# Kernel optimization log

Measured on AMD Instinct MI355X. Metric: run time of the kernel, lower is better.

## Reference

```python
import jax, jax.numpy as jnp
import numpy as np

MARGIN = 0.1
N, CHOICES = 16384, 2048


def setup_inputs() -> dict:
    key = jax.random.key(0)
    k1, k2 = jax.random.split(key)
    cossim = jax.random.normal(k1, (N, CHOICES), dtype=jnp.float32)
    correct_idx = jax.random.randint(k2, (N,), 0, CHOICES)
    # one-hot int64 target: exactly one 1 per row, as the module expects
    target = (jnp.arange(CHOICES)[None, :] == correct_idx[:, None]).astype(jnp.int64)
    return {"cossim": cossim, "target": target}


def reference(cossim, target):
    # correct index / similarity per row
    correct_idx = jnp.argmax(target, axis=1)                                   # [N]
    correct_sim = jnp.take_along_axis(cossim, correct_idx[:, None], axis=1)    # [N,1]
    # hinge over all choices, then zero out the correct-choice term
    hinge = jnp.maximum(MARGIN + cossim - correct_sim, 0.0)                    # [N,C]
    hinge = jnp.where(target == 1, 0.0, hinge)
    loss = jnp.sum(hinge, axis=1)                                              # [N]
    return jnp.mean(loss)
```

## Files before the change

### kernel.cpp

```cpp
#include <hip/hip_runtime.h>
#include <hip/hip_bf16.h>


constexpr int   kC      = 2048;
constexpr float kMargin = 0.1f;

__global__ __launch_bounds__(256) void max_margin_kernel(
    const float* __restrict__ cossim,
    const int*   __restrict__ target,
    float*       __restrict__ out,
    int nrows, float inv_n)
{
    const int lane          = threadIdx.x & 63;
    const int wave_in_block = threadIdx.x >> 6;
    const int wave          = blockIdx.x * 4 + wave_in_block;
    const int nwaves        = gridDim.x * 4;

    float acc = 0.0f;

    for (int row = wave; row < nrows; row += nwaves) {
        const size_t row_off = (size_t)row * kC;

        const int4* t = (const int4*)(target + row_off);
        float sim = -3.0e38f;
        #pragma unroll
        for (int k = 0; k < kC / (64 * 4); ++k) {
            int4 v   = t[lane + k * 64];
            int base = (lane + k * 64) * 4;
            if (v.x == 1) sim = cossim[row_off + base + 0];
            if (v.y == 1) sim = cossim[row_off + base + 1];
            if (v.z == 1) sim = cossim[row_off + base + 2];
            if (v.w == 1) sim = cossim[row_off + base + 3];
        }
        #pragma unroll
        for (int off = 32; off > 0; off >>= 1)
            sim = fmaxf(sim, __shfl_xor(sim, off));

        const float4* c = (const float4*)(cossim + row_off);
        float s = 0.0f;
        #pragma unroll
        for (int k = 0; k < kC / (64 * 4); ++k) {
            float4 v = c[lane + k * 64];
            s += fmaxf(kMargin + v.x - sim, 0.0f);
            s += fmaxf(kMargin + v.y - sim, 0.0f);
            s += fmaxf(kMargin + v.z - sim, 0.0f);
            s += fmaxf(kMargin + v.w - sim, 0.0f);
        }
        if (lane == 0) s -= kMargin;
        acc += s;
    }

    #pragma unroll
    for (int off = 32; off > 0; off >>= 1)
        acc += __shfl_xor(acc, off);

    __shared__ float ws[4];
    if (lane == 0) ws[wave_in_block] = acc;
    __syncthreads();
    if (threadIdx.x == 0) {
        float b = ws[0] + ws[1] + ws[2] + ws[3];
        atomicAdd(out, b * inv_n);
    }
}

extern "C" void kernel_launch(void* const* d_in, const int* in_sizes, int n_in,
                              void* d_out, int out_size, void* d_ws, size_t ws_size,
                              hipStream_t stream)
{
    const float* cossim = (const float*)d_in[0];
    const int*   target = (const int*)d_in[1];
    float*       out    = (float*)d_out;

    const int nrows = in_sizes[0] / kC;

    hipMemsetAsync(out, 0, sizeof(float), stream);

    const int blocks = (nrows + 3) / 4;
    max_margin_kernel<<<blocks, 256, 0, stream>>>(cossim, target, out,
                                                  nrows, 1.0f / (float)nrows);
}
```

Before: 278.0 us.

## Split correct-sim lookup and hinge sum into two streaming kernels

The fused per-row kernel is split in two. The first is a grid-stride kernel that scans the one-hot target as int4 vectors and writes each row's correct similarity into workspace. The second computes the hinge sum with one wave per row, using that precomputed value. This removes the dependency inside each wave between scanning the target and loading the cossim row, so both streams can be read with more memory-level parallelism. The cost is an extra kernel launch and a small workspace round trip.

```diff
diff --git a/kernel.cpp b/kernel.cpp
--- a/kernel.cpp
+++ b/kernel.cpp
@@ -5,39 +5,44 @@
 constexpr int   kC      = 2048;
 constexpr float kMargin = 0.1f;
 
-__global__ __launch_bounds__(256) void max_margin_kernel(
+__global__ __launch_bounds__(256) void find_correct_sim(
     const float* __restrict__ cossim,
-    const int*   __restrict__ target,
+    const int4*  __restrict__ target4,
+    float*       __restrict__ correct_sim,
+    int total4)
+{
+    const int stride = gridDim.x * blockDim.x;
+    for (int f = blockIdx.x * blockDim.x + threadIdx.x; f < total4; f += stride) {
+        int4 v = target4[f];
+        if ((v.x | v.y | v.z | v.w) != 0) {
+            int base = f << 2;
+            int row  = base >> 11;
+            int col  = base & (kC - 1);
+            const float* crow = cossim + (size_t)row * kC;
+            float s;
+            if      (v.x == 1) s = crow[col + 0];
+            else if (v.y == 1) s = crow[col + 1];
+            else if (v.z == 1) s = crow[col + 2];
+            else               s = crow[col + 3];
+            correct_sim[row] = s;
+        }
+    }
+}
+
+__global__ __launch_bounds__(256) void hinge_sum(
+    const float* __restrict__ cossim,
+    const float* __restrict__ correct_sim,
     float*       __restrict__ out,
     int nrows, float inv_n)
 {
     const int lane          = threadIdx.x & 63;
     const int wave_in_block = threadIdx.x >> 6;
-    const int wave          = blockIdx.x * 4 + wave_in_block;
-    const int nwaves        = gridDim.x * 4;
+    const int row           = blockIdx.x * 4 + wave_in_block;
 
-    float acc = 0.0f;
-
-    for (int row = wave; row < nrows; row += nwaves) {
-        const size_t row_off = (size_t)row * kC;
-
-        const int4* t = (const int4*)(target + row_off);
-        float sim = -3.0e38f;
-        #pragma unroll
-        for (int k = 0; k < kC / (64 * 4); ++k) {
-            int4 v   = t[lane + k * 64];
-            int base = (lane + k * 64) * 4;
-            if (v.x == 1) sim = cossim[row_off + base + 0];
-            if (v.y == 1) sim = cossim[row_off + base + 1];
-            if (v.z == 1) sim = cossim[row_off + base + 2];
-            if (v.w == 1) sim = cossim[row_off + base + 3];
-        }
-        #pragma unroll
-        for (int off = 32; off > 0; off >>= 1)
-            sim = fmaxf(sim, __shfl_xor(sim, off));
-
-        const float4* c = (const float4*)(cossim + row_off);
-        float s = 0.0f;
+    float s = 0.0f;
+    if (row < nrows) {
+        const float sim = correct_sim[row];
+        const float4* c = (const float4*)(cossim + (size_t)row * kC);
         #pragma unroll
         for (int k = 0; k < kC / (64 * 4); ++k) {
             float4 v = c[lane + k * 64];
@@ -47,15 +52,14 @@
             s += fmaxf(kMargin + v.w - sim, 0.0f);
         }
         if (lane == 0) s -= kMargin;
-        acc += s;
     }
 
     #pragma unroll
     for (int off = 32; off > 0; off >>= 1)
-        acc += __shfl_xor(acc, off);
+        s += __shfl_xor(s, off);
 
     __shared__ float ws[4];
-    if (lane == 0) ws[wave_in_block] = acc;
+    if (lane == 0) ws[wave_in_block] = s;
     __syncthreads();
     if (threadIdx.x == 0) {
         float b = ws[0] + ws[1] + ws[2] + ws[3];
@@ -70,12 +74,16 @@
     const float* cossim = (const float*)d_in[0];
     const int*   target = (const int*)d_in[1];
     float*       out    = (float*)d_out;
+    float*       csim   = (float*)d_ws;
 
-    const int nrows = in_sizes[0] / kC;
+    const int nrows  = in_sizes[0] / kC;
+    const int total4 = in_sizes[1] / 4;
 
     hipMemsetAsync(out, 0, sizeof(float), stream);
 
-    const int blocks = (nrows + 3) / 4;
-    max_margin_kernel<<<blocks, 256, 0, stream>>>(cossim, target, out,
-                                                  nrows, 1.0f / (float)nrows);
+    find_correct_sim<<<2048, 256, 0, stream>>>(cossim, (const int4*)target,
+                                               csim, total4);
+
+    hinge_sum<<<(nrows + 3) / 4, 256, 0, stream>>>(cossim, csim, out,
+                                                   nrows, 1.0f / (float)nrows);
 }
```

Result: slower. 289.4 us (+4.1%).

## Process one row per block and load target and cossim together in one pass

Applied to the files above, without the earlier changes.

Each 256-thread block now handles a single row. Every thread loads its target and cossim vectors at the same time, and the correct similarity is shared through LDS after a barrier, so cossim is read once instead of twice. This replaces the one-wave-per-row two-pass scheme and exposes more memory parallelism per row. In exchange it adds a block barrier and issues one atomic per row, 16384 atomics on a single address.

```diff
diff --git a/kernel.cpp b/kernel.cpp
--- a/kernel.cpp
+++ b/kernel.cpp
@@ -5,59 +5,56 @@
 constexpr int   kC      = 2048;
 constexpr float kMargin = 0.1f;
 
-__global__ __launch_bounds__(256) void max_margin_kernel(
+__global__ __launch_bounds__(256) void max_margin_fused(
     const float* __restrict__ cossim,
     const int*   __restrict__ target,
     float*       __restrict__ out,
-    int nrows, float inv_n)
+    float inv_n)
 {
-    const int lane          = threadIdx.x & 63;
-    const int wave_in_block = threadIdx.x >> 6;
-    const int wave          = blockIdx.x * 4 + wave_in_block;
-    const int nwaves        = gridDim.x * 4;
+    const int row = blockIdx.x;
+    const int tid = threadIdx.x;
+    const size_t base = (size_t)row * kC;
 
-    float acc = 0.0f;
+    const int4*   t4 = (const int4*)(target + base);
+    const float4* c4 = (const float4*)(cossim + base);
 
-    for (int row = wave; row < nrows; row += nwaves) {
-        const size_t row_off = (size_t)row * kC;
+    int4   t0 = t4[tid];
+    int4   t1 = t4[tid + 256];
+    float4 c0 = c4[tid];
+    float4 c1 = c4[tid + 256];
 
-        const int4* t = (const int4*)(target + row_off);
-        float sim = -3.0e38f;
-        #pragma unroll
-        for (int k = 0; k < kC / (64 * 4); ++k) {
-            int4 v   = t[lane + k * 64];
-            int base = (lane + k * 64) * 4;
-            if (v.x == 1) sim = cossim[row_off + base + 0];
-            if (v.y == 1) sim = cossim[row_off + base + 1];
-            if (v.z == 1) sim = cossim[row_off + base + 2];
-            if (v.w == 1) sim = cossim[row_off + base + 3];
-        }
-        #pragma unroll
-        for (int off = 32; off > 0; off >>= 1)
-            sim = fmaxf(sim, __shfl_xor(sim, off));
+    __shared__ float s_sim;
 
-        const float4* c = (const float4*)(cossim + row_off);
-        float s = 0.0f;
-        #pragma unroll
-        for (int k = 0; k < kC / (64 * 4); ++k) {
-            float4 v = c[lane + k * 64];
-            s += fmaxf(kMargin + v.x - sim, 0.0f);
-            s += fmaxf(kMargin + v.y - sim, 0.0f);
-            s += fmaxf(kMargin + v.z - sim, 0.0f);
-            s += fmaxf(kMargin + v.w - sim, 0.0f);
-        }
-        if (lane == 0) s -= kMargin;
-        acc += s;
-    }
+    if (t0.x | t0.y | t0.z | t0.w)
+        s_sim = t0.x ? c0.x : (t0.y ? c0.y : (t0.z ? c0.z : c0.w));
+    if (t1.x | t1.y | t1.z | t1.w)
+        s_sim = t1.x ? c1.x : (t1.y ? c1.y : (t1.z ? c1.z : c1.w));
+    __syncthreads();
+
+    const float sim = s_sim;
+
+    float s = 0.0f;
+    s += fmaxf(kMargin + c0.x - sim, 0.0f);
+    s += fmaxf(kMargin + c0.y - sim, 0.0f);
+    s += fmaxf(kMargin + c0.z - sim, 0.0f);
+    s += fmaxf(kMargin + c0.w - sim, 0.0f);
+    s += fmaxf(kMargin + c1.x - sim, 0.0f);
+    s += fmaxf(kMargin + c1.y - sim, 0.0f);
+    s += fmaxf(kMargin + c1.z - sim, 0.0f);
+    s += fmaxf(kMargin + c1.w - sim, 0.0f);
+
+    if (tid == 0) s -= kMargin;
 
     #pragma unroll
-    for (int off = 32; off > 0; off >>= 1)
-        acc += __shfl_xor(acc, off);
+    for (int o = 32; o > 0; o >>= 1)
+        s += __shfl_xor(s, o);
 
     __shared__ float ws[4];
-    if (lane == 0) ws[wave_in_block] = acc;
+    const int lane = tid & 63;
+    const int wib  = tid >> 6;
+    if (lane == 0) ws[wib] = s;
     __syncthreads();
-    if (threadIdx.x == 0) {
+    if (tid == 0) {
         float b = ws[0] + ws[1] + ws[2] + ws[3];
         atomicAdd(out, b * inv_n);
     }
@@ -75,7 +72,6 @@
 
     hipMemsetAsync(out, 0, sizeof(float), stream);
 
-    const int blocks = (nrows + 3) / 4;
-    max_margin_kernel<<<blocks, 256, 0, stream>>>(cossim, target, out,
-                                                  nrows, 1.0f / (float)nrows);
+    max_margin_fused<<<nrows, 256, 0, stream>>>(cossim, target, out,
+                                                1.0f / (float)nrows);
 }
```

Result: slower. 398.0 us (+43.2%).
